# Kernel tuning notes

Measured on AMD Instinct MI355X. Metric: run time of the kernel, lower is better.

The kernel has to match this reference:

```python
import jax, jax.numpy as jnp
import numpy as np

EPS = 1e-06

def phi(x):
    # canonical linear-attention feature map: elu(x) + 1 (positive features)
    return jax.nn.elu(x) + 1.0

def setup_inputs() -> dict:
    key = jax.random.key(0)
    kq, kk, kv = jax.random.split(key, 3)
    B, H, S, D = 4, 16, 4096, 64
    query = jax.random.normal(kq, (B, H, S, D), dtype=jnp.float32)
    k = jax.random.normal(kk, (B, H, S, D), dtype=jnp.float32)
    value = jax.random.normal(kv, (B, H, S, D), dtype=jnp.float32)
    attention_mask = jnp.ones((B, S), dtype=jnp.float32)
    return {"query": query, "key": k, "value": value, "attention_mask": attention_mask}

def reference(query, key, value, attention_mask):
    B, H, S, D = query.shape
    q = query / jnp.sqrt(jnp.asarray(D, query.dtype))
    phi_q = phi(q)                                   # [b,h,n,d]
    phi_k = phi(key)                                 # [b,h,n,d]
    mask = attention_mask[:, None, :, None].astype(phi_k.dtype)  # [b,1,n,1]
    phi_k = phi_k * mask
    kv_term = jnp.einsum('bhnd,bhnv->bhdv', phi_k, value)        # [b,h,d,v]
    output = jnp.einsum('bhnd,bhdv->bhnv', phi_q, kv_term)       # [b,h,n,v]
    k_one = jnp.sum(phi_k, axis=2)                               # [b,h,d] == phi_k @ masked ones
    normalizer = jnp.einsum('bhnd,bhd->bhn', phi_q, k_one)[..., None]  # [b,h,n,1]
    return output / (normalizer + EPS)
```

## Files before the change

### kernel.cpp

```cpp
#include <hip/hip_runtime.h>

typedef unsigned short ushort_t;
typedef unsigned int uint32;
typedef __bf16 bf16x8 __attribute__((ext_vector_type(8)));
typedef float f32x4 __attribute__((ext_vector_type(4)));

#define NB 4
#define NH 16
#define NS 4096
#define ND 64
#define NBH 64
#define EPSF 1e-6f

#define CH1 16
#define ROWS1 (NS / CH1)
#define P2R 128
#define LDJ 72
#define LDJW 36
#define BTSZ (80 * 64)

__device__ __forceinline__ float phi_f(float x) {
    return x > 0.0f ? x + 1.0f : __expf(x);
}
__device__ __forceinline__ ushort_t bf16_rn(float x) {
    uint32 u = __float_as_uint(x);
    uint32 r = (u + 0x7FFFu + ((u >> 16) & 1u)) >> 16;
    return (ushort_t)r;
}
__device__ __forceinline__ void split2(float x, ushort_t& h, ushort_t& l) {
    h = bf16_rn(x);
    float hf = __uint_as_float(((uint32)h) << 16);
    l = bf16_rn(x - hf);
}
union FragP { ushort_t s[8]; bf16x8 v; };
__device__ __forceinline__ bf16x8 ld_frag(const ushort_t* arr, int widx) {
    return *(const bf16x8*)((const uint32*)arr + widx);
}
__device__ __forceinline__ f32x4 mfma16(bf16x8 a, bf16x8 b, f32x4 c) {
    return __builtin_amdgcn_mfma_f32_16x16x32_bf16(a, b, c, 0, 0, 0);
}

template<bool PART>
__global__ __launch_bounds__(256, 4)
void la_pass1(const float* __restrict__ Kin, const float* __restrict__ Vin,
              const float* __restrict__ Min, float* __restrict__ okv,
              float* __restrict__ ok1)
{
    const int t  = threadIdx.x;
    const int cx = blockIdx.x;
    const int bh = blockIdx.y;
    const int bb = bh >> 4;
    const float* Kb = Kin + (long long)bh * NS * ND;
    const float* Vb = Vin + (long long)bh * NS * ND;
    const float* Mb = Min + (long long)bb * NS;

    __shared__ __align__(16) ushort_t skh[64 * LDJ], skl[64 * LDJ];
    __shared__ __align__(16) ushort_t svh[64 * LDJ], svl[64 * LDJ];

    const int p  = t & 31;
    const int c0 = (t >> 5) * 8;
    const int wv = t >> 6;
    const int m  = t & 15;
    const int q  = (t & 63) >> 4;

    const f32x4 zf = {0.f, 0.f, 0.f, 0.f};
    f32x4 acc0 = zf, acc1 = zf, acc2 = zf, acc3 = zf;
    float k1loc[8] = {0.f,0.f,0.f,0.f,0.f,0.f,0.f,0.f};

    const int s0 = cx * ROWS1;

    float4 ka, kb2, kc, kd, va, vb2, vc, vd;
    float m0, m1;
#define LOADT(tt) { \
        const int r0_ = s0 + (tt) * 64 + 2 * p; \
        const float* kp_ = Kb + (long long)r0_ * ND + c0; \
        const float* vp_ = Vb + (long long)r0_ * ND + c0; \
        ka  = *(const float4*)kp_;        kb2 = *(const float4*)(kp_ + 4); \
        kc  = *(const float4*)(kp_ + ND); kd  = *(const float4*)(kp_ + ND + 4); \
        va  = *(const float4*)vp_;        vb2 = *(const float4*)(vp_ + 4); \
        vc  = *(const float4*)(vp_ + ND); vd  = *(const float4*)(vp_ + ND + 4); \
        m0 = Mb[r0_]; m1 = Mb[r0_ + 1]; }

    LOADT(0);

    for (int tile = 0; tile < ROWS1 / 64; ++tile) {
        const float kr0[8] = {ka.x,ka.y,ka.z,ka.w,kb2.x,kb2.y,kb2.z,kb2.w};
        const float kr1[8] = {kc.x,kc.y,kc.z,kc.w,kd.x,kd.y,kd.z,kd.w};
        const float vr0[8] = {va.x,va.y,va.z,va.w,vb2.x,vb2.y,vb2.z,vb2.w};
        const float vr1[8] = {vc.x,vc.y,vc.z,vc.w,vd.x,vd.y,vd.z,vd.w};
        uint32 wkh[8], wkl[8], wvh[8], wvl[8];
        #pragma unroll
        for (int i = 0; i < 8; ++i) {
            const float x0 = phi_f(kr0[i]) * m0;
            const float x1 = phi_f(kr1[i]) * m1;
            k1loc[i] += x0 + x1;
            ushort_t h0, l0, h1, l1;
            split2(x0, h0, l0); split2(x1, h1, l1);
            wkh[i] = (uint32)h0 | ((uint32)h1 << 16);
            wkl[i] = (uint32)l0 | ((uint32)l1 << 16);
            split2(vr0[i], h0, l0); split2(vr1[i], h1, l1);
            wvh[i] = (uint32)h0 | ((uint32)h1 << 16);
            wvl[i] = (uint32)l0 | ((uint32)l1 << 16);
        }
        __syncthreads();
        #pragma unroll
        for (int i = 0; i < 8; ++i) {
            const int widx = (c0 + i) * LDJW + p;
            ((uint32*)skh)[widx] = wkh[i];
            ((uint32*)skl)[widx] = wkl[i];
            ((uint32*)svh)[widx] = wvh[i];
            ((uint32*)svl)[widx] = wvl[i];
        }
        if (tile + 1 < ROWS1 / 64) LOADT(tile + 1);
        __syncthreads();
        #pragma unroll
        for (int ks = 0; ks < 2; ++ks) {
            const int fo = ks * 16 + q * 4;
            const bf16x8 ah = ld_frag(skh, (16 * wv + m) * LDJW + fo);
            const bf16x8 al = ld_frag(skl, (16 * wv + m) * LDJW + fo);
            {
                const bf16x8 fbh = ld_frag(svh, (0 + m) * LDJW + fo);
                const bf16x8 fbl = ld_frag(svl, (0 + m) * LDJW + fo);
                acc0 = mfma16(al, fbh, acc0); acc0 = mfma16(ah, fbl, acc0); acc0 = mfma16(ah, fbh, acc0);
            }
            {
                const bf16x8 fbh = ld_frag(svh, (16 + m) * LDJW + fo);
                const bf16x8 fbl = ld_frag(svl, (16 + m) * LDJW + fo);
                acc1 = mfma16(al, fbh, acc1); acc1 = mfma16(ah, fbl, acc1); acc1 = mfma16(ah, fbh, acc1);
            }
            {
                const bf16x8 fbh = ld_frag(svh, (32 + m) * LDJW + fo);
                const bf16x8 fbl = ld_frag(svl, (32 + m) * LDJW + fo);
                acc2 = mfma16(al, fbh, acc2); acc2 = mfma16(ah, fbl, acc2); acc2 = mfma16(ah, fbh, acc2);
            }
            {
                const bf16x8 fbh = ld_frag(svh, (48 + m) * LDJW + fo);
                const bf16x8 fbl = ld_frag(svl, (48 + m) * LDJW + fo);
                acc3 = mfma16(al, fbh, acc3); acc3 = mfma16(ah, fbl, acc3); acc3 = mfma16(ah, fbh, acc3);
            }
        }
    }
#undef LOADT

    const int dbase = 16 * wv + q * 4;
    if (PART) {
        float* outp = okv + (long long)(bh * CH1 + cx) * (ND * ND);
        #pragma unroll
        for (int i = 0; i < 4; ++i) {
            outp[(dbase + i) * ND +  0 + m] = acc0[i];
            outp[(dbase + i) * ND + 16 + m] = acc1[i];
            outp[(dbase + i) * ND + 32 + m] = acc2[i];
            outp[(dbase + i) * ND + 48 + m] = acc3[i];
        }
    } else {
        float* outp = okv + (long long)bh * (ND * ND);
        #pragma unroll
        for (int i = 0; i < 4; ++i) {
            atomicAdd(&outp[(dbase + i) * ND +  0 + m], acc0[i]);
            atomicAdd(&outp[(dbase + i) * ND + 16 + m], acc1[i]);
            atomicAdd(&outp[(dbase + i) * ND + 32 + m], acc2[i]);
            atomicAdd(&outp[(dbase + i) * ND + 48 + m], acc3[i]);
        }
    }
    __syncthreads();
    float* red = (float*)skh;
    #pragma unroll
    for (int i = 0; i < 8; ++i) red[(c0 + i) * 33 + p] = k1loc[i];
    __syncthreads();
    if (t < 64) {
        float s = 0.f;
        #pragma unroll
        for (int pp = 0; pp < 32; ++pp) s += red[t * 33 + pp];
        if (PART) ok1[(bh * CH1 + cx) * ND + t] = s;
        else      atomicAdd(&ok1[bh * ND + t], s);
    }
}

__global__ __launch_bounds__(256)
void la_reduce(const float* __restrict__ pkv, const float* __restrict__ pk1,
               ushort_t* __restrict__ BTh, ushort_t* __restrict__ BTl)
{
    const int t = threadIdx.x;
    const int bh = blockIdx.x;
    const float4* src = (const float4*)(pkv + (long long)bh * CH1 * ND * ND);
    float4 a[4];
    #pragma unroll
    for (int i = 0; i < 4; ++i) { a[i].x = 0.f; a[i].y = 0.f; a[i].z = 0.f; a[i].w = 0.f; }
    for (int c = 0; c < CH1; ++c) {
        #pragma unroll
        for (int i = 0; i < 4; ++i) {
            const float4 v = src[c * 1024 + t + 256 * i];
            a[i].x += v.x; a[i].y += v.y; a[i].z += v.z; a[i].w += v.w;
        }
    }
    ushort_t* oh = BTh + (long long)bh * BTSZ;
    ushort_t* ol = BTl + (long long)bh * BTSZ;
    #pragma unroll
    for (int i = 0; i < 4; ++i) {
        const int e4 = t + 256 * i;
        const int d  = e4 >> 4;
        const int v0 = (e4 & 15) * 4;
        const float vals[4] = {a[i].x, a[i].y, a[i].z, a[i].w};
        #pragma unroll
        for (int j = 0; j < 4; ++j) {
            ushort_t h, l; split2(vals[j], h, l);
            oh[(v0 + j) * ND + d] = h;
            ol[(v0 + j) * ND + d] = l;
        }
    }
    if (t < ND) {
        float s = 0.f;
        for (int c = 0; c < CH1; ++c) s += pk1[(bh * CH1 + c) * ND + t];
        ushort_t h, l; split2(s, h, l);
        oh[64 * ND + t] = h; ol[64 * ND + t] = l;
    }
    for (int z = t; z < 15 * 64; z += 256) { oh[65 * ND + z] = 0; ol[65 * ND + z] = 0; }
}

__global__ __launch_bounds__(256)
void la_convert(const float* __restrict__ kv, const float* __restrict__ k1,
                ushort_t* __restrict__ BTh, ushort_t* __restrict__ BTl)
{
    const int t = threadIdx.x;
    const int bh = blockIdx.x;
    const float* kvb = kv + (long long)bh * ND * ND;
    ushort_t* oh = BTh + (long long)bh * BTSZ;
    ushort_t* ol = BTl + (long long)bh * BTSZ;
    for (int e = t; e < ND * ND; e += 256) {
        const int d = e >> 6, v = e & 63;
        ushort_t h, l; split2(kvb[e], h, l);
        oh[v * ND + d] = h; ol[v * ND + d] = l;
    }
    if (t < ND) { ushort_t h, l; split2(k1[bh * ND + t], h, l); oh[64 * ND + t] = h; ol[64 * ND + t] = l; }
    for (int z = t; z < 15 * 64; z += 256) { oh[65 * ND + z] = 0; ol[65 * ND + z] = 0; }
}

__global__ __launch_bounds__(256, 4)
void la_pass2(const float* __restrict__ Qin, const ushort_t* __restrict__ BTh,
              const ushort_t* __restrict__ BTl, float* __restrict__ Out)
{
    const int t  = threadIdx.x;
    const int bh = blockIdx.y;
    const int s0 = blockIdx.x * P2R;
    const long long base = (long long)bh * NS * ND;
    const int wv = t >> 6;
    const int m  = t & 15;
    const int q  = (t & 63) >> 4;
    const int lane = t & 63;
    const ushort_t* Bh = BTh + (long long)bh * BTSZ;
    const ushort_t* Bl = BTl + (long long)bh * BTSZ;

    bf16x8 aH[2][2], aL[2][2];
    #pragma unroll
    for (int mtl = 0; mtl < 2; ++mtl) {
        const int row = s0 + 32 * wv + 16 * mtl + m;
        const float* qp = Qin + base + (long long)row * ND;
        #pragma unroll
        for (int ks = 0; ks < 2; ++ks) {
            const float4 x0 = *(const float4*)(qp + ks * 32 + q * 8);
            const float4 x1 = *(const float4*)(qp + ks * 32 + q * 8 + 4);
            const float xs[8] = {x0.x,x0.y,x0.z,x0.w,x1.x,x1.y,x1.z,x1.w};
            FragP fh, fl;
            #pragma unroll
            for (int i = 0; i < 8; ++i) {
                ushort_t h, l; split2(phi_f(xs[i] * 0.125f), h, l);
                fh.s[i] = h; fl.s[i] = l;
            }
            aH[mtl][ks] = fh.v; aL[mtl][ks] = fl.v;
        }
    }

    const f32x4 zf = {0.f, 0.f, 0.f, 0.f};
    f32x4 acc[2][5];
    #pragma unroll
    for (int a = 0; a < 2; ++a)
        #pragma unroll
        for (int b = 0; b < 5; ++b) acc[a][b] = zf;

    #pragma unroll
    for (int ks = 0; ks < 2; ++ks) {
        #pragma unroll
        for (int nt = 0; nt < 5; ++nt) {
            const int bo = (16 * nt + m) * ND + ks * 32 + q * 8;
            const bf16x8 fbh = *(const bf16x8*)(Bh + bo);
            const bf16x8 fbl = *(const bf16x8*)(Bl + bo);
            acc[0][nt] = mfma16(aL[0][ks], fbh, acc[0][nt]);
            acc[0][nt] = mfma16(aH[0][ks], fbl, acc[0][nt]);
            acc[0][nt] = mfma16(aH[0][ks], fbh, acc[0][nt]);
            acc[1][nt] = mfma16(aL[1][ks], fbh, acc[1][nt]);
            acc[1][nt] = mfma16(aH[1][ks], fbl, acc[1][nt]);
            acc[1][nt] = mfma16(aH[1][ks], fbh, acc[1][nt]);
        }
    }

    float* outb = Out + base;
    #pragma unroll
    for (int mtl = 0; mtl < 2; ++mtl) {
        const int rbase = s0 + 32 * wv + 16 * mtl + q * 4;
        #pragma unroll
        for (int i = 0; i < 4; ++i) {
            const float nv = __shfl(acc[mtl][4][i], lane & 48, 64);
            const float rn = 1.0f / (nv + EPSF);
            const long long ro = (long long)(rbase + i) * ND;
            outb[ro +  0 + m] = acc[mtl][0][i] * rn;
            outb[ro + 16 + m] = acc[mtl][1][i] * rn;
            outb[ro + 32 + m] = acc[mtl][2][i] * rn;
            outb[ro + 48 + m] = acc[mtl][3][i] * rn;
        }
    }
}

extern "C" void kernel_launch(void* const* d_in, const int* in_sizes, int n_in,
                              void* d_out, int out_size, void* d_ws, size_t ws_size,
                              hipStream_t stream)
{
    const float* Q = (const float*)d_in[0];
    const float* K = (const float*)d_in[1];
    const float* V = (const float*)d_in[2];
    const float* M = (const float*)d_in[3];
    float* Out = (float*)d_out;

    const size_t partf = (size_t)NBH * CH1 * ND * ND;
    const size_t pk1f  = (size_t)NBH * CH1 * ND;
    const size_t kvf   = (size_t)NBH * ND * ND;
    const size_t k1f   = (size_t)NBH * ND;
    const size_t btu   = (size_t)NBH * BTSZ;
    const size_t need  = (partf + pk1f) * sizeof(float) + 2 * btu * sizeof(ushort_t);

    if (ws_size >= need) {
        float* PKV = (float*)d_ws;
        float* PK1 = PKV + partf;
        ushort_t* BThp = (ushort_t*)(PK1 + pk1f);
        ushort_t* BTlp = BThp + btu;
        la_pass1<true><<<dim3(CH1, NBH), dim3(256), 0, stream>>>(K, V, M, PKV, PK1);
        la_reduce<<<dim3(NBH), dim3(256), 0, stream>>>(PKV, PK1, BThp, BTlp);
        la_pass2<<<dim3(NS / P2R, NBH), dim3(256), 0, stream>>>(Q, BThp, BTlp, Out);
    } else {
        float* KVb = (float*)d_ws;
        float* K1b = KVb + kvf;
        ushort_t* BThp = (ushort_t*)(K1b + k1f);
        ushort_t* BTlp = BThp + btu;
        hipMemsetAsync(d_ws, 0, (kvf + k1f) * sizeof(float), stream);
        la_pass1<false><<<dim3(CH1, NBH), dim3(256), 0, stream>>>(K, V, M, KVb, K1b);
        la_convert<<<dim3(NBH), dim3(256), 0, stream>>>(KVb, K1b, BThp, BTlp);
        la_pass2<<<dim3(NS / P2R, NBH), dim3(256), 0, stream>>>(Q, BThp, BTlp, Out);
    }
}
```

Measured before the change: 249.1 us.

## Double pass1 threads and halve pass2 rows per block to raise parallelism

Pass1 now runs 512 threads per block, so each thread loads and converts 4 columns instead of 8, and each wave owns two of the 64x64 KV output tiles instead of four. Pass2 handles 64 query rows per block with one 16-row tile per wave, giving twice as many blocks with fewer live registers, and raises the occupancy hint. The aim is more waves in flight to hide global memory latency in both kernels. The cost is more blocks re-reading the BT matrices in pass2 and more duplicated LDS fragment reads in pass1.

```diff
diff --git a/kernel.cpp b/kernel.cpp
--- a/kernel.cpp
+++ b/kernel.cpp
@@ -14,7 +14,7 @@
 
 #define CH1 16
 #define ROWS1 (NS / CH1)
-#define P2R 128
+#define P2R 64
 #define LDJ 72
 #define LDJW 36
 #define BTSZ (80 * 64)
@@ -41,7 +41,7 @@
 }
 
 template<bool PART>
-__global__ __launch_bounds__(256, 4)
+__global__ __launch_bounds__(512, 8)
 void la_pass1(const float* __restrict__ Kin, const float* __restrict__ Vin,
               const float* __restrict__ Min, float* __restrict__ okv,
               float* __restrict__ ok1)
@@ -58,114 +58,94 @@
     __shared__ __align__(16) ushort_t svh[64 * LDJ], svl[64 * LDJ];
 
     const int p  = t & 31;
-    const int c0 = (t >> 5) * 8;
+    const int c0 = (t >> 5) * 4;
     const int wv = t >> 6;
+    const int ds = wv >> 1;
+    const int nb = (wv & 1) * 2;
     const int m  = t & 15;
     const int q  = (t & 63) >> 4;
 
     const f32x4 zf = {0.f, 0.f, 0.f, 0.f};
-    f32x4 acc0 = zf, acc1 = zf, acc2 = zf, acc3 = zf;
-    float k1loc[8] = {0.f,0.f,0.f,0.f,0.f,0.f,0.f,0.f};
+    f32x4 acc0 = zf, acc1 = zf;
+    float k1loc[4] = {0.f, 0.f, 0.f, 0.f};
 
     const int s0 = cx * ROWS1;
 
-    float4 ka, kb2, kc, kd, va, vb2, vc, vd;
+    float4 ka, kc, va, vc;
     float m0, m1;
 #define LOADT(tt) { \
         const int r0_ = s0 + (tt) * 64 + 2 * p; \
         const float* kp_ = Kb + (long long)r0_ * ND + c0; \
         const float* vp_ = Vb + (long long)r0_ * ND + c0; \
-        ka  = *(const float4*)kp_;        kb2 = *(const float4*)(kp_ + 4); \
-        kc  = *(const float4*)(kp_ + ND); kd  = *(const float4*)(kp_ + ND + 4); \
-        va  = *(const float4*)vp_;        vb2 = *(const float4*)(vp_ + 4); \
-        vc  = *(const float4*)(vp_ + ND); vd  = *(const float4*)(vp_ + ND + 4); \
+        ka = *(const float4*)kp_;  kc = *(const float4*)(kp_ + ND); \
+        va = *(const float4*)vp_;  vc = *(const float4*)(vp_ + ND); \
         m0 = Mb[r0_]; m1 = Mb[r0_ + 1]; }
 
     LOADT(0);
 
     for (int tile = 0; tile < ROWS1 / 64; ++tile) {
-        const float kr0[8] = {ka.x,ka.y,ka.z,ka.w,kb2.x,kb2.y,kb2.z,kb2.w};
-        const float kr1[8] = {kc.x,kc.y,kc.z,kc.w,kd.x,kd.y,kd.z,kd.w};
-        const float vr0[8] = {va.x,va.y,va.z,va.w,vb2.x,vb2.y,vb2.z,vb2.w};
-        const float vr1[8] = {vc.x,vc.y,vc.z,vc.w,vd.x,vd.y,vd.z,vd.w};
-        uint32 wkh[8], wkl[8], wvh[8], wvl[8];
-        #pragma unroll
-        for (int i = 0; i < 8; ++i) {
-            const float x0 = phi_f(kr0[i]) * m0;
-            const float x1 = phi_f(kr1[i]) * m1;
-            k1loc[i] += x0 + x1;
-            ushort_t h0, l0, h1, l1;
-            split2(x0, h0, l0); split2(x1, h1, l1);
-            wkh[i] = (uint32)h0 | ((uint32)h1 << 16);
-            wkl[i] = (uint32)l0 | ((uint32)l1 << 16);
-            split2(vr0[i], h0, l0); split2(vr1[i], h1, l1);
-            wvh[i] = (uint32)h0 | ((uint32)h1 << 16);
-            wvl[i] = (uint32)l0 | ((uint32)l1 << 16);
-        }
         __syncthreads();
-        #pragma unroll
-        for (int i = 0; i < 8; ++i) {
-            const int widx = (c0 + i) * LDJW + p;
-            ((uint32*)skh)[widx] = wkh[i];
-            ((uint32*)skl)[widx] = wkl[i];
-            ((uint32*)svh)[widx] = wvh[i];
-            ((uint32*)svl)[widx] = wvl[i];
+        {
+            const float kr0[4] = {ka.x, ka.y, ka.z, ka.w};
+            const float kr1[4] = {kc.x, kc.y, kc.z, kc.w};
+            const float vr0[4] = {va.x, va.y, va.z, va.w};
+            const float vr1[4] = {vc.x, vc.y, vc.z, vc.w};
+            #pragma unroll
+            for (int i = 0; i < 4; ++i) {
+                const float x0 = phi_f(kr0[i]) * m0;
+                const float x1 = phi_f(kr1[i]) * m1;
+                k1loc[i] += x0 + x1;
+                ushort_t h0, l0, h1, l1;
+                split2(x0, h0, l0); split2(x1, h1, l1);
+                const int widx = (c0 + i) * LDJW + p;
+                ((uint32*)skh)[widx] = (uint32)h0 | ((uint32)h1 << 16);
+                ((uint32*)skl)[widx] = (uint32)l0 | ((uint32)l1 << 16);
+                split2(vr0[i], h0, l0); split2(vr1[i], h1, l1);
+                ((uint32*)svh)[widx] = (uint32)h0 | ((uint32)h1 << 16);
+                ((uint32*)svl)[widx] = (uint32)l0 | ((uint32)l1 << 16);
+            }
         }
         if (tile + 1 < ROWS1 / 64) LOADT(tile + 1);
         __syncthreads();
         #pragma unroll
         for (int ks = 0; ks < 2; ++ks) {
             const int fo = ks * 16 + q * 4;
-            const bf16x8 ah = ld_frag(skh, (16 * wv + m) * LDJW + fo);
-            const bf16x8 al = ld_frag(skl, (16 * wv + m) * LDJW + fo);
+            const bf16x8 ah = ld_frag(skh, (16 * ds + m) * LDJW + fo);
+            const bf16x8 al = ld_frag(skl, (16 * ds + m) * LDJW + fo);
             {
-                const bf16x8 fbh = ld_frag(svh, (0 + m) * LDJW + fo);
-                const bf16x8 fbl = ld_frag(svl, (0 + m) * LDJW + fo);
+                const bf16x8 fbh = ld_frag(svh, (16 * (nb + 0) + m) * LDJW + fo);
+                const bf16x8 fbl = ld_frag(svl, (16 * (nb + 0) + m) * LDJW + fo);
                 acc0 = mfma16(al, fbh, acc0); acc0 = mfma16(ah, fbl, acc0); acc0 = mfma16(ah, fbh, acc0);
             }
             {
-                const bf16x8 fbh = ld_frag(svh, (16 + m) * LDJW + fo);
-                const bf16x8 fbl = ld_frag(svl, (16 + m) * LDJW + fo);
+                const bf16x8 fbh = ld_frag(svh, (16 * (nb + 1) + m) * LDJW + fo);
+                const bf16x8 fbl = ld_frag(svl, (16 * (nb + 1) + m) * LDJW + fo);
                 acc1 = mfma16(al, fbh, acc1); acc1 = mfma16(ah, fbl, acc1); acc1 = mfma16(ah, fbh, acc1);
             }
-            {
-                const bf16x8 fbh = ld_frag(svh, (32 + m) * LDJW + fo);
-                const bf16x8 fbl = ld_frag(svl, (32 + m) * LDJW + fo);
-                acc2 = mfma16(al, fbh, acc2); acc2 = mfma16(ah, fbl, acc2); acc2 = mfma16(ah, fbh, acc2);
-            }
-            {
-                const bf16x8 fbh = ld_frag(svh, (48 + m) * LDJW + fo);
-                const bf16x8 fbl = ld_frag(svl, (48 + m) * LDJW + fo);
-                acc3 = mfma16(al, fbh, acc3); acc3 = mfma16(ah, fbl, acc3); acc3 = mfma16(ah, fbh, acc3);
-            }
         }
     }
 #undef LOADT
 
-    const int dbase = 16 * wv + q * 4;
+    const int dbase = 16 * ds + q * 4;
     if (PART) {
         float* outp = okv + (long long)(bh * CH1 + cx) * (ND * ND);
         #pragma unroll
         for (int i = 0; i < 4; ++i) {
-            outp[(dbase + i) * ND +  0 + m] = acc0[i];
-            outp[(dbase + i) * ND + 16 + m] = acc1[i];
-            outp[(dbase + i) * ND + 32 + m] = acc2[i];
-            outp[(dbase + i) * ND + 48 + m] = acc3[i];
+            outp[(dbase + i) * ND + 16 * (nb + 0) + m] = acc0[i];
+            outp[(dbase + i) * ND + 16 * (nb + 1) + m] = acc1[i];
         }
     } else {
         float* outp = okv + (long long)bh * (ND * ND);
         #pragma unroll
         for (int i = 0; i < 4; ++i) {
-            atomicAdd(&outp[(dbase + i) * ND +  0 + m], acc0[i]);
-            atomicAdd(&outp[(dbase + i) * ND + 16 + m], acc1[i]);
-            atomicAdd(&outp[(dbase + i) * ND + 32 + m], acc2[i]);
-            atomicAdd(&outp[(dbase + i) * ND + 48 + m], acc3[i]);
+            atomicAdd(&outp[(dbase + i) * ND + 16 * (nb + 0) + m], acc0[i]);
+            atomicAdd(&outp[(dbase + i) * ND + 16 * (nb + 1) + m], acc1[i]);
         }
     }
     __syncthreads();
     float* red = (float*)skh;
     #pragma unroll
-    for (int i = 0; i < 8; ++i) red[(c0 + i) * 33 + p] = k1loc[i];
+    for (int i = 0; i < 4; ++i) red[(c0 + i) * 33 + p] = k1loc[i];
     __syncthreads();
     if (t < 64) {
         float s = 0.f;
@@ -235,7 +215,7 @@
     for (int z = t; z < 15 * 64; z += 256) { oh[65 * ND + z] = 0; ol[65 * ND + z] = 0; }
 }
 
-__global__ __launch_bounds__(256, 4)
+__global__ __launch_bounds__(256, 6)
 void la_pass2(const float* __restrict__ Qin, const ushort_t* __restrict__ BTh,
               const ushort_t* __restrict__ BTl, float* __restrict__ Out)
 {
@@ -250,63 +230,59 @@
     const ushort_t* Bh = BTh + (long long)bh * BTSZ;
     const ushort_t* Bl = BTl + (long long)bh * BTSZ;
 
-    bf16x8 aH[2][2], aL[2][2];
-    #pragma unroll
-    for (int mtl = 0; mtl < 2; ++mtl) {
-        const int row = s0 + 32 * wv + 16 * mtl + m;
+    bf16x8 aH[2], aL[2];
+    {
+        const int row = s0 + 16 * wv + m;
         const float* qp = Qin + base + (long long)row * ND;
+        float4 x0[2], x1[2];
         #pragma unroll
         for (int ks = 0; ks < 2; ++ks) {
-            const float4 x0 = *(const float4*)(qp + ks * 32 + q * 8);
-            const float4 x1 = *(const float4*)(qp + ks * 32 + q * 8 + 4);
-            const float xs[8] = {x0.x,x0.y,x0.z,x0.w,x1.x,x1.y,x1.z,x1.w};
+            x0[ks] = *(const float4*)(qp + ks * 32 + q * 8);
+            x1[ks] = *(const float4*)(qp + ks * 32 + q * 8 + 4);
+        }
+        #pragma unroll
+        for (int ks = 0; ks < 2; ++ks) {
+            const float xs[8] = {x0[ks].x, x0[ks].y, x0[ks].z, x0[ks].w,
+                                 x1[ks].x, x1[ks].y, x1[ks].z, x1[ks].w};
             FragP fh, fl;
             #pragma unroll
             for (int i = 0; i < 8; ++i) {
                 ushort_t h, l; split2(phi_f(xs[i] * 0.125f), h, l);
                 fh.s[i] = h; fl.s[i] = l;
             }
-            aH[mtl][ks] = fh.v; aL[mtl][ks] = fl.v;
+            aH[ks] = fh.v; aL[ks] = fl.v;
         }
     }
 
     const f32x4 zf = {0.f, 0.f, 0.f, 0.f};
-    f32x4 acc[2][5];
-    #pragma unroll
-    for (int a = 0; a < 2; ++a)
-        #pragma unroll
-        for (int b = 0; b < 5; ++b) acc[a][b] = zf;
-
-    #pragma unroll
-    for (int ks = 0; ks < 2; ++ks) {
-        #pragma unroll
-        for (int nt = 0; nt < 5; ++nt) {
+    f32x4 acc[5];
+    #pragma unroll
+    for (int b = 0; b < 5; ++b) acc[b] = zf;
+
+    #pragma unroll
+    for (int nt = 0; nt < 5; ++nt) {
+        #pragma unroll
+        for (int ks = 0; ks < 2; ++ks) {
             const int bo = (16 * nt + m) * ND + ks * 32 + q * 8;
             const bf16x8 fbh = *(const bf16x8*)(Bh + bo);
             const bf16x8 fbl = *(const bf16x8*)(Bl + bo);
-            acc[0][nt] = mfma16(aL[0][ks], fbh, acc[0][nt]);
-            acc[0][nt] = mfma16(aH[0][ks], fbl, acc[0][nt]);
-            acc[0][nt] = mfma16(aH[0][ks], fbh, acc[0][nt]);
-            acc[1][nt] = mfma16(aL[1][ks], fbh, acc[1][nt]);
-            acc[1][nt] = mfma16(aH[1][ks], fbl, acc[1][nt]);
-            acc[1][nt] = mfma16(aH[1][ks], fbh, acc[1][nt]);
+            acc[nt] = mfma16(aL[ks], fbh, acc[nt]);
+            acc[nt] = mfma16(aH[ks], fbl, acc[nt]);
+            acc[nt] = mfma16(aH[ks], fbh, acc[nt]);
         }
     }
 
     float* outb = Out + base;
-    #pragma unroll
-    for (int mtl = 0; mtl < 2; ++mtl) {
-        const int rbase = s0 + 32 * wv + 16 * mtl + q * 4;
-        #pragma unroll
-        for (int i = 0; i < 4; ++i) {
-            const float nv = __shfl(acc[mtl][4][i], lane & 48, 64);
-            const float rn = 1.0f / (nv + EPSF);
-            const long long ro = (long long)(rbase + i) * ND;
-            outb[ro +  0 + m] = acc[mtl][0][i] * rn;
-            outb[ro + 16 + m] = acc[mtl][1][i] * rn;
-            outb[ro + 32 + m] = acc[mtl][2][i] * rn;
-            outb[ro + 48 + m] = acc[mtl][3][i] * rn;
-        }
+    const int rbase = s0 + 16 * wv + q * 4;
+    #pragma unroll
+    for (int i = 0; i < 4; ++i) {
+        const float nv = __shfl(acc[4][i], lane & 48, 64);
+        const float rn = 1.0f / (nv + EPSF);
+        const long long ro = (long long)(rbase + i) * ND;
+        outb[ro +  0 + m] = acc[0][i] * rn;
+        outb[ro + 16 + m] = acc[1][i] * rn;
+        outb[ro + 32 + m] = acc[2][i] * rn;
+        outb[ro + 48 + m] = acc[3][i] * rn;
     }
 }
 
@@ -332,7 +308,7 @@
         float* PK1 = PKV + partf;
         ushort_t* BThp = (ushort_t*)(PK1 + pk1f);
         ushort_t* BTlp = BThp + btu;
-        la_pass1<true><<<dim3(CH1, NBH), dim3(256), 0, stream>>>(K, V, M, PKV, PK1);
+        la_pass1<true><<<dim3(CH1, NBH), dim3(512), 0, stream>>>(K, V, M, PKV, PK1);
         la_reduce<<<dim3(NBH), dim3(256), 0, stream>>>(PKV, PK1, BThp, BTlp);
         la_pass2<<<dim3(NS / P2R, NBH), dim3(256), 0, stream>>>(Q, BThp, BTlp, Out);
     } else {
@@ -341,7 +317,7 @@
         ushort_t* BThp = (ushort_t*)(K1b + k1f);
         ushort_t* BTlp = BThp + btu;
         hipMemsetAsync(d_ws, 0, (kvf + k1f) * sizeof(float), stream);
-        la_pass1<false><<<dim3(CH1, NBH), dim3(256), 0, stream>>>(K, V, M, KVb, K1b);
+        la_pass1<false><<<dim3(CH1, NBH), dim3(512), 0, stream>>>(K, V, M, KVb, K1b);
         la_convert<<<dim3(NBH), dim3(256), 0, stream>>>(KVb, K1b, BThp, BTlp);
         la_pass2<<<dim3(NS / P2R, NBH), dim3(256), 0, stream>>>(Q, BThp, BTlp, Out);
     }
```

After: 264.9 us. 6.4% more time.
